# Kernel tuning notes

Hardware: AMD Instinct MI355X
Metric: run time of the kernel (lower is better)

Reference implementation:

```python
import jax, jax.numpy as jnp
import numpy as np

ALPHA = 0.5
GAMMA = 0.01
TOP_K = 5
B, T, C = 2048, 8192, 1  # C must be 1 for amp_loss's grouped conv1d to be valid


def _ashift_loss(inp, tgt):
    _, t_len, _ = inp.shape
    sm = jax.nn.softmax(inp - tgt, axis=1)                      # [B,T,C]
    return jnp.mean(jnp.sum(jnp.abs(1.0 / t_len - sm), axis=1, keepdims=True))


def _phase_loss(inp, tgt, top_k=TOP_K):
    inp_f = jnp.fft.rfft(inp, axis=1)                           # [B,Tf,C] complex
    tgt_f = jnp.fft.rfft(tgt, axis=1)
    b, tf_len, c = tgt_f.shape
    amp = jnp.abs(tgt_f).at[:, 0, :].set(0.0)                   # zero DC bin
    # top-k magnitudes along freq axis (per batch, per channel)
    _, idx = jax.lax.top_k(jnp.transpose(amp, (0, 2, 1)), top_k)  # [B,C,k]
    top = jnp.transpose(idx, (0, 2, 1))                         # [B,k,C]
    # boolean mask: True everywhere except top-k freq bins (per column)
    freqs = jnp.arange(tf_len)
    mask = ~jnp.any(freqs[None, :, None, None] == top[:, None, :, :], axis=2)  # [B,Tf,C]
    # replicate torch row-major boolean-mask flatten + view(B, Tf-k, C):
    flat = mask.reshape(b, tf_len * c)
    order = jnp.argsort(~flat, axis=1, stable=True)             # kept (True) positions first, in row-major order
    keep = order[:, : (tf_len - top_k) * c]                     # flat (t*C + c') positions
    non_top = (keep // c).reshape(b, tf_len - top_k, c)         # stored value is the freq index t
    dom = jnp.take_along_axis(tgt_f, top, axis=1) - jnp.take_along_axis(inp_f, top, axis=1)
    domain_loss = jnp.mean(jnp.sqrt(jnp.sum(jnp.abs(dom) ** 2, axis=1)))
    gath = jnp.take_along_axis(inp_f, non_top, axis=1)          # [B,Tf-k,C]
    nondomain_loss = jnp.mean(jnp.sqrt(jnp.sum(jnp.abs(gath) ** 2, axis=1, keepdims=True)))
    return domain_loss + nondomain_loss


def _amp_loss(inp, tgt):
    # Valid only for C==1: conv1d([B,1,T], weight=[B,1,T], groups=1) -> [B,B,1]
    # out[b,o] = sum_t tgt[b,t] * flip(kernel)[o,t]
    t2 = tgt[:, :, 0]                                           # [B,T]
    i2 = inp[:, :, 0]
    flip_diff = t2[:, ::-1] - i2[:, ::-1]                       # flip(target) - flip(input)
    diff = jnp.einsum('bt,ot->bo', t2, flip_diff)               # self_corr - cross_corr, [B,B]
    # torch.norm(p=2) over the singleton dim == abs
    return jnp.mean(jnp.abs(diff))


def setup_inputs() -> dict:
    key = jax.random.key(0)
    k1, k2 = jax.random.split(key)
    inp = jax.random.normal(k1, (B, T, C), dtype=jnp.float32)
    tgt = jax.random.normal(k2, (B, T, C), dtype=jnp.float32)
    return {"input": inp, "target": tgt}


def reference(input, target):
    return (ALPHA * _ashift_loss(input, target)
            + (1.0 - ALPHA) * _phase_loss(input, target)
            + GAMMA * _amp_loss(input, target))
```

## Files before the change

kernel.cpp:

```cpp
#include <hip/hip_runtime.h>
#include <hip/hip_bf16.h>
#include <math.h>

#define B_N 2048
#define T_N 8192
#define NFFT 4096
#define TF_LEN 4097
#define TOPK 5
#define KSPLIT 4
#define GBK 64

#define ZIDX(n) ((n) + ((n) >> 4) + ((n) >> 8))
#define ZPAD (NFFT + (NFFT >> 4) + (NFFT >> 8))

typedef float f32x4 __attribute__((ext_vector_type(4)));
typedef __bf16 bf16x8 __attribute__((ext_vector_type(8)));
typedef unsigned short ushort_t;

__device__ __forceinline__ void gload_lds16(const ushort_t* g, ushort_t* l) {
    __builtin_amdgcn_global_load_lds(
        (const __attribute__((address_space(1))) void*)g,
        (__attribute__((address_space(3))) void*)l,
        16, 0, 0);
}

__device__ __forceinline__ float wave_reduce_sum(float v) {
    for (int o = 32; o >= 1; o >>= 1) v += __shfl_xor(v, o, 64);
    return v;
}
__device__ __forceinline__ float wave_reduce_max(float v) {
    for (int o = 32; o >= 1; o >>= 1) v = fmaxf(v, __shfl_xor(v, o, 64));
    return v;
}

__device__ __forceinline__ ushort_t f2bf(float x) {
    __hip_bfloat16 h = __float2bfloat16(x);
    return *reinterpret_cast<ushort_t*>(&h);
}

__device__ __forceinline__ float2 cis_rev(float rev) {
    return make_float2(__builtin_amdgcn_cosf(rev), __builtin_amdgcn_sinf(rev));
}
__device__ __forceinline__ float2 cmulf(float2 a, float2 b) {
    return make_float2(a.x * b.x - a.y * b.y, a.x * b.y + a.y * b.x);
}

__device__ __forceinline__ void gen_pows(float2 w1, float2 tw[16]) {
    tw[1] = w1;
    tw[2] = cmulf(w1, w1);
    tw[3] = cmulf(tw[2], w1);
    tw[4] = cmulf(tw[2], tw[2]);
    tw[5] = cmulf(tw[4], w1);
    tw[6] = cmulf(tw[4], tw[2]);
    tw[7] = cmulf(tw[4], tw[3]);
    tw[8] = cmulf(tw[4], tw[4]);
    tw[9] = cmulf(tw[8], w1);
    tw[10] = cmulf(tw[8], tw[2]);
    tw[11] = cmulf(tw[8], tw[3]);
    tw[12] = cmulf(tw[8], tw[4]);
    tw[13] = cmulf(tw[8], tw[5]);
    tw[14] = cmulf(tw[8], tw[6]);
    tw[15] = cmulf(tw[8], tw[7]);
}

__global__ __launch_bounds__(256) void init_kernel(float* acc, float* Cpart, int nzbuf) {
    if (blockIdx.x == 0 && threadIdx.x < 4) acc[threadIdx.x] = 0.0f;
    if (nzbuf == 1) {
        size_t idx = ((size_t)blockIdx.x * 256 + threadIdx.x) * 4;
        *reinterpret_cast<f32x4*>(&Cpart[idx]) = (f32x4){0.f, 0.f, 0.f, 0.f};
    }
}

__device__ __forceinline__ void dft4(float2 x0, float2 x1, float2 x2, float2 x3,
                                     float2* y0, float2* y1, float2* y2, float2* y3) {
    float2 t0 = make_float2(x0.x + x2.x, x0.y + x2.y);
    float2 t1 = make_float2(x0.x - x2.x, x0.y - x2.y);
    float2 t2 = make_float2(x1.x + x3.x, x1.y + x3.y);
    float2 t3 = make_float2(x1.x - x3.x, x1.y - x3.y);
    *y0 = make_float2(t0.x + t2.x, t0.y + t2.y);
    *y2 = make_float2(t0.x - t2.x, t0.y - t2.y);
    *y1 = make_float2(t1.x + t3.y, t1.y - t3.x);
    *y3 = make_float2(t1.x - t3.y, t1.y + t3.x);
}

__device__ __forceinline__ void dft16(float2 X[16]) {
    float2 G[16];
    dft4(X[0], X[4], X[8],  X[12], &G[0],  &G[1],  &G[2],  &G[3]);
    dft4(X[1], X[5], X[9],  X[13], &G[4],  &G[5],  &G[6],  &G[7]);
    dft4(X[2], X[6], X[10], X[14], &G[8],  &G[9],  &G[10], &G[11]);
    dft4(X[3], X[7], X[11], X[15], &G[12], &G[13], &G[14], &G[15]);
    const float C1 = 0.9238795325112867f, S1 = 0.3826834323650898f;
    const float R2 = 0.7071067811865476f;
    G[5]  = cmulf(G[5],  make_float2(C1, -S1));
    G[6]  = cmulf(G[6],  make_float2(R2, -R2));
    G[7]  = cmulf(G[7],  make_float2(S1, -C1));
    G[9]  = cmulf(G[9],  make_float2(R2, -R2));
    { float2 g = G[10]; G[10] = make_float2(g.y, -g.x); }
    G[11] = cmulf(G[11], make_float2(-R2, -R2));
    G[13] = cmulf(G[13], make_float2(S1, -C1));
    G[14] = cmulf(G[14], make_float2(-R2, -R2));
    G[15] = cmulf(G[15], make_float2(-C1, S1));
    dft4(G[0], G[4], G[8],  G[12], &X[0], &X[4], &X[8],  &X[12]);
    dft4(G[1], G[5], G[9],  G[13], &X[1], &X[5], &X[9],  &X[13]);
    dft4(G[2], G[6], G[10], G[14], &X[2], &X[6], &X[10], &X[14]);
    dft4(G[3], G[7], G[11], G[15], &X[3], &X[7], &X[11], &X[15]);
}

__device__ __forceinline__ void rfft_bin(const float2* Zs, int k, float* orr, float* oi) {
    int kk = k & (NFFT - 1);
    int nk = (NFFT - k) & (NFFT - 1);
    float2 zk = Zs[ZIDX(kk)], znk = Zs[ZIDX(nk)];
    float xer = 0.5f * (zk.x + znk.x);
    float xei = 0.5f * (zk.y - znk.y);
    float xo_r = 0.5f * (zk.y + znk.y);
    float xo_i = -0.5f * (zk.x - znk.x);
    float2 w = cis_rev((float)k * (-1.0f / (float)T_N));
    *orr = xer + w.x * xo_r - w.y * xo_i;
    *oi = xei + w.x * xo_i + w.y * xo_r;
}

__global__ __launch_bounds__(256) void fused_row_kernel(const float* __restrict__ inp,
                                                        const float* __restrict__ tgt,
                                                        ushort_t* __restrict__ Abf,
                                                        ushort_t* __restrict__ Bbf,
                                                        float* acc) {
    __shared__ float2 Zs[ZPAD];
    __shared__ float red[12];
    __shared__ float wv[2][4];
    __shared__ int wi[2][4];
    __shared__ float2 tgtF[TOPK];
    __shared__ float rscratch[64];

    int b = blockIdx.x;
    int tid = threadIdx.x;
    int lane = tid & 63, wid = tid >> 6;
    const float* tp = tgt + (size_t)b * T_N;
    const float* ip = inp + (size_t)b * T_N;
    ushort_t* Ab = Abf + (size_t)b * T_N;
    ushort_t* Bb = Bbf + (size_t)b * T_N;

    float4 trv[8];
#pragma unroll
    for (int i = 0; i < 8; i++) {
        int q = tid + 256 * i;
        trv[i] = *reinterpret_cast<const float4*>(&tp[4 * q]);
        ushort4 ua;
        ua.x = f2bf(trv[i].x); ua.y = f2bf(trv[i].y);
        ua.z = f2bf(trv[i].z); ua.w = f2bf(trv[i].w);
        *reinterpret_cast<ushort4*>(&Ab[4 * q]) = ua;
        int m0 = 2 * q, m1 = 2 * q + 1;
        int p0 = ((m0 & 15) << 8) | (m0 & 0x0F0) | (m0 >> 8);
        int p1 = ((m1 & 15) << 8) | (m1 & 0x0F0) | (m1 >> 8);
        Zs[ZIDX(p0)] = make_float2(trv[i].x, trv[i].y);
        Zs[ZIDX(p1)] = make_float2(trv[i].z, trv[i].w);
    }

    float4 irv[8], dv[8];
#pragma unroll
    for (int i = 0; i < 8; i++) {
        int q = tid + 256 * i;
        irv[i] = *reinterpret_cast<const float4*>(&ip[4 * q]);
        dv[i] = make_float4(irv[i].x - trv[i].x, irv[i].y - trv[i].y,
                            irv[i].z - trv[i].z, irv[i].w - trv[i].w);
        ushort4 ub;
        ub.x = f2bf(-dv[i].w); ub.y = f2bf(-dv[i].z);
        ub.z = f2bf(-dv[i].y); ub.w = f2bf(-dv[i].x);
        uint2 p = *reinterpret_cast<uint2*>(&ub);
        p.x = __shfl_xor(p.x, 63, 64);
        p.y = __shfl_xor(p.y, 63, 64);
        int o = lane + 64 * (31 - wid - 4 * i);
        *reinterpret_cast<uint2*>(&Bb[4 * o]) = p;
    }

    {
        float lmax = -1e30f;
#pragma unroll
        for (int i = 0; i < 8; i++)
            lmax = fmaxf(lmax, fmaxf(fmaxf(dv[i].x, dv[i].y), fmaxf(dv[i].z, dv[i].w)));
        lmax = wave_reduce_max(lmax);
        if (lane == 0) red[wid] = lmax;
        __syncthreads();
        float mx = fmaxf(fmaxf(red[0], red[1]), fmaxf(red[2], red[3]));
        float lsum = 0.0f;
#pragma unroll
        for (int i = 0; i < 8; i++) {
            dv[i].x = __expf(dv[i].x - mx);
            dv[i].y = __expf(dv[i].y - mx);
            dv[i].z = __expf(dv[i].z - mx);
            dv[i].w = __expf(dv[i].w - mx);
            lsum += (dv[i].x + dv[i].y) + (dv[i].z + dv[i].w);
        }
        lsum = wave_reduce_sum(lsum);
        if (lane == 0) red[4 + wid] = lsum;
        __syncthreads();
        float Z = (red[4] + red[5]) + (red[6] + red[7]);
        float inv = 1.0f / Z;
        const float u = 1.0f / (float)T_N;
        float labs = 0.0f;
#pragma unroll
        for (int i = 0; i < 8; i++) {
            labs += fabsf(u - dv[i].x * inv) + fabsf(u - dv[i].y * inv) +
                    fabsf(u - dv[i].z * inv) + fabsf(u - dv[i].w * inv);
        }
        labs = wave_reduce_sum(labs);
        if (lane == 0) red[8 + wid] = labs;
        __syncthreads();
        if (tid == 0)
            atomicAdd(acc + 0, (red[8] + red[9]) + (red[10] + red[11]));
    }

    {
        float2 X[16];
        int base = tid * 16;
#pragma unroll
        for (int r = 0; r < 16; r++) X[r] = Zs[ZIDX(base + r)];
        dft16(X);
#pragma unroll
        for (int r = 0; r < 16; r++) Zs[ZIDX(base + r)] = X[r];
    }
    __syncthreads();
    {
        float2 X[16];
        int j = tid & 15;
        int base = (tid >> 4) * 256 + j;
#pragma unroll
        for (int r = 0; r < 16; r++) X[r] = Zs[ZIDX(base + 16 * r)];
        float2 tw[16];
        gen_pows(cis_rev(-(float)j * (1.0f / 256.0f)), tw);
#pragma unroll
        for (int r = 1; r < 16; r++) X[r] = cmulf(X[r], tw[r]);
        dft16(X);
#pragma unroll
        for (int r = 0; r < 16; r++) Zs[ZIDX(base + 16 * r)] = X[r];
    }
    __syncthreads();
    {
        float2 X[16];
#pragma unroll
        for (int r = 0; r < 16; r++) X[r] = Zs[ZIDX(tid + 256 * r)];
        float2 tw[16];
        gen_pows(cis_rev(-(float)tid * (1.0f / 4096.0f)), tw);
#pragma unroll
        for (int r = 1; r < 16; r++) X[r] = cmulf(X[r], tw[r]);
        dft16(X);
#pragma unroll
        for (int r = 0; r < 16; r++) Zs[ZIDX(tid + 256 * r)] = X[r];
    }
    __syncthreads();

    float av[16];
    float aN = -3.0f;
    {
        const float CC[16] = {
            1.0f, 0.9807852804032304f, 0.9238795325112867f, 0.8314696123025452f,
            0.7071067811865476f, 0.5555702330196022f, 0.3826834323650898f,
            0.1950903220161283f, 0.0f, -0.1950903220161283f, -0.3826834323650898f,
            -0.5555702330196022f, -0.7071067811865476f, -0.8314696123025452f,
            -0.9238795325112867f, -0.9807852804032304f};
        const float SS[16] = {
            0.0f, -0.1950903220161283f, -0.3826834323650898f, -0.5555702330196022f,
            -0.7071067811865476f, -0.8314696123025452f, -0.9238795325112867f,
            -0.9807852804032304f, -1.0f, -0.9807852804032304f, -0.9238795325112867f,
            -0.8314696123025452f, -0.7071067811865476f, -0.5555702330196022f,
            -0.3826834323650898f, -0.1950903220161283f};
        float2 rot0 = cis_rev(-(float)tid * (1.0f / (float)T_N));
#pragma unroll
        for (int i = 0; i < 16; i++) {
            int k = tid + 256 * i;
            if (i == 0 && tid == 0) {
                av[i] = -1.0f;
            } else {
                float2 rot = cmulf(rot0, make_float2(CC[i], SS[i]));
                int nk = (NFFT - k) & (NFFT - 1);
                float2 zk = Zs[ZIDX(k & (NFFT - 1))], znk = Zs[ZIDX(nk)];
                float xer = 0.5f * (zk.x + znk.x);
                float xei = 0.5f * (zk.y - znk.y);
                float xo_r = 0.5f * (zk.y + znk.y);
                float xo_i = -0.5f * (zk.x - znk.x);
                float xr = xer + rot.x * xo_r - rot.y * xo_i;
                float xi = xei + rot.x * xo_i + rot.y * xo_r;
                av[i] = xr * xr + xi * xi;
            }
        }
        if (tid == 0) {
            float2 z0 = Zs[ZIDX(0)];
            float v = z0.x - z0.y;
            aN = v * v;
        }
    }

    int fqa[TOPK];
#pragma unroll
    for (int r = 0; r < TOPK; r++) {
        float bv = -3.0f;
        int bi = TF_LEN;
#pragma unroll
        for (int i = 0; i < 16; i++) {
            float a = av[i];
            if (a > bv) { bv = a; bi = tid + 256 * i; }
        }
        if (aN > bv) { bv = aN; bi = 4096; }
        for (int o = 1; o < 64; o <<= 1) {
            float ov = __shfl_xor(bv, o, 64);
            int oi = __shfl_xor(bi, o, 64);
            if (ov > bv || (ov == bv && oi < bi)) { bv = ov; bi = oi; }
        }
        if (lane == 0) { wv[r & 1][wid] = bv; wi[r & 1][wid] = bi; }
        __syncthreads();
        float fv = wv[r & 1][0];
        int fi = wi[r & 1][0];
#pragma unroll
        for (int w2 = 1; w2 < 4; w2++) {
            float cv = wv[r & 1][w2];
            int ci = wi[r & 1][w2];
            if (cv > fv || (cv == fv && ci < fi)) { fv = cv; fi = ci; }
        }
        fqa[r] = fi;
        if (fi == 4096) {
            if (tid == 0) aN = -2.0f;
        } else if ((fi & 255) == tid) {
            int slot = fi >> 8;
#pragma unroll
            for (int i = 0; i < 16; i++)
                if (i == slot) av[i] = -2.0f;
        }
    }

    if (tid < TOPK) {
        int myf = fqa[0];
        if (tid == 1) myf = fqa[1];
        if (tid == 2) myf = fqa[2];
        if (tid == 3) myf = fqa[3];
        if (tid == 4) myf = fqa[4];
        float xr, xi;
        rfft_bin(Zs, myf, &xr, &xi);
        tgtF[tid] = make_float2(xr, xi);
    }
    __syncthreads();

    float2 cur[TOPK], wr[TOPK];
    float pre[TOPK][4], pim[TOPK][4];
#pragma unroll
    for (int q = 0; q < TOPK; q++) {
        int f = fqa[q];
        cur[q] = cis_rev(-(float)((f * 4 * tid) & (T_N - 1)) * (1.0f / (float)T_N));
        wr[q] = cis_rev(-(float)((f * 1024) & (T_N - 1)) * (1.0f / (float)T_N));
#pragma unroll
        for (int c = 0; c < 4; c++) { pre[q][c] = 0.0f; pim[q][c] = 0.0f; }
    }
    float E = 0.0f, sev = 0.0f, sod = 0.0f;
#pragma unroll
    for (int i = 0; i < 8; i++) {
        float4 v = irv[i];
        E = fmaf(v.x, v.x, E); sev += v.x;
        E = fmaf(v.y, v.y, E); sod += v.y;
        E = fmaf(v.z, v.z, E); sev += v.z;
        E = fmaf(v.w, v.w, E); sod += v.w;
#pragma unroll
        for (int q = 0; q < TOPK; q++) {
            pre[q][0] = fmaf(v.x, cur[q].x, pre[q][0]);
            pim[q][0] = fmaf(v.x, cur[q].y, pim[q][0]);
            pre[q][1] = fmaf(v.y, cur[q].x, pre[q][1]);
            pim[q][1] = fmaf(v.y, cur[q].y, pim[q][1]);
            pre[q][2] = fmaf(v.z, cur[q].x, pre[q][2]);
            pim[q][2] = fmaf(v.z, cur[q].y, pim[q][2]);
            pre[q][3] = fmaf(v.w, cur[q].x, pre[q][3]);
            pim[q][3] = fmaf(v.w, cur[q].y, pim[q][3]);
            cur[q] = cmulf(cur[q], wr[q]);
        }
    }
    float re[TOPK], im[TOPK];
#pragma unroll
    for (int q = 0; q < TOPK; q++) {
        float2 wcq = cis_rev(-(float)fqa[q] * (1.0f / (float)T_N));
        float tr = pre[q][3], ti = pim[q][3];
        float ur = pre[q][2] + (wcq.x * tr - wcq.y * ti);
        float ui = pim[q][2] + (wcq.x * ti + wcq.y * tr);
        float vr = pre[q][1] + (wcq.x * ur - wcq.y * ui);
        float vi = pim[q][1] + (wcq.x * ui + wcq.y * ur);
        re[q] = pre[q][0] + (wcq.x * vr - wcq.y * vi);
        im[q] = pim[q][0] + (wcq.x * vi + wcq.y * vr);
    }

    float vals[13] = {re[0], im[0], re[1], im[1], re[2], im[2], re[3], im[3],
                      re[4], im[4], E, sev + sod, sev - sod};
#pragma unroll
    for (int i = 0; i < 13; i++) {
        float v = wave_reduce_sum(vals[i]);
        if (lane == 0) rscratch[wid * 13 + i] = v;
    }
    __syncthreads();
    if (tid == 0) {
        float tot[13];
        for (int i = 0; i < 13; i++)
            tot[i] = rscratch[i] + rscratch[13 + i] + rscratch[26 + i] + rscratch[39 + i];
        float dsum = 0, isum = 0;
        for (int q = 0; q < TOPK; q++) {
            float rr = tot[2 * q], ii = tot[2 * q + 1];
            float dr = tgtF[q].x - rr, di = tgtF[q].y - ii;
            dsum += dr * dr + di * di;
            isum += rr * rr + ii * ii;
        }
        float Ee = tot[10], X0v = tot[11], Xhv = tot[12];
        float S_all = 0.5f * ((float)T_N * Ee + X0v * X0v + Xhv * Xhv);
        float val = sqrtf(dsum) + sqrtf(fmaxf(S_all - isum, 0.0f));
        atomicAdd(acc + 1, val);
    }
}

__global__ __launch_bounds__(512, 2) void gemm_kernel(const ushort_t* __restrict__ A,
                                                      const ushort_t* __restrict__ Bm,
                                                      float* __restrict__ Cpart,
                                                      int nzbuf) {
    __shared__ __align__(16) ushort_t lds[2][4][128 * 64];
    int tid = threadIdx.x;
    int bid = blockIdx.x;
    int swz = ((bid & 7) << 5) | (bid >> 3);
    int bx = swz & 7, by = (swz >> 3) & 7, bz = swz >> 6;
    int row0 = bx * 256, col0 = by * 256;
    const int KC = T_N / KSPLIT;
    const int NT = KC / GBK;
    const int NIT = NT / 2;
    int kbase = bz * KC;

    int w = tid >> 6, lane = tid & 63;
    int wm = w >> 2, wn = w & 3;
    int lr = lane & 15, kq = lane >> 4;

    f32x4 accf[8][4];
#pragma unroll
    for (int mi = 0; mi < 8; mi++)
#pragma unroll
        for (int ni = 0; ni < 4; ni++) accf[mi][ni] = (f32x4){0.f, 0.f, 0.f, 0.f};

    int strow = tid >> 3;
    int scb = (tid & 7) ^ (strow & 7);
    const ushort_t* gA0 = A + (size_t)(row0 + strow) * T_N + kbase + scb * 8;
    const ushort_t* gA1 = A + (size_t)(row0 + 128 + strow) * T_N + kbase + scb * 8;
    const ushort_t* gB0 = Bm + (size_t)(col0 + strow) * T_N + kbase + scb * 8;
    const ushort_t* gB1 = Bm + (size_t)(col0 + 128 + strow) * T_N + kbase + scb * 8;
    const size_t SUB = (size_t)64 * T_N;

    int rb0 = lr * 64 + ((kq ^ (lr & 7)) << 3);
    int rb1 = lr * 64 + (((4 + kq) ^ (lr & 7)) << 3);

#define SA_(s, buf, kt)                                                        \
    do {                                                                       \
        gload_lds16(gA0 + (s) * SUB + (size_t)(kt) * GBK, &lds[buf][0][(s) * 4096 + tid * 8]); \
        gload_lds16(gA1 + (s) * SUB + (size_t)(kt) * GBK, &lds[buf][1][(s) * 4096 + tid * 8]); \
    } while (0)
#define SB_(rg, buf, kt)                                                       \
    do {                                                                       \
        const ushort_t* g_ = ((rg) == 2) ? gB0 : gB1;                          \
        gload_lds16(g_ + (size_t)(kt) * GBK, &lds[buf][rg][tid * 8]);          \
        gload_lds16(g_ + SUB + (size_t)(kt) * GBK, &lds[buf][rg][4096 + tid * 8]); \
    } while (0)

#define PHASE(BUF, QM, QN, VMN, STAGE_STMT)                                    \
    do {                                                                       \
        asm volatile("s_waitcnt vmcnt(" #VMN ")" ::: "memory");                \
        const ushort_t* Ab_ = &lds[BUF][wm][0];                                \
        const ushort_t* Bb_ = &lds[BUF][2 + (wn >> 1)][(wn & 1) * 4096];       \
        bf16x8 a_[4][2], b_[2][2];                                             \
        _Pragma("unroll") for (int m_ = 0; m_ < 4; m_++) {                     \
            a_[m_][0] = *reinterpret_cast<const bf16x8*>(Ab_ + (QM) * 4096 + m_ * 1024 + rb0); \
            a_[m_][1] = *reinterpret_cast<const bf16x8*>(Ab_ + (QM) * 4096 + m_ * 1024 + rb1); \
        }                                                                      \
        _Pragma("unroll") for (int n_ = 0; n_ < 2; n_++) {                     \
            b_[n_][0] = *reinterpret_cast<const bf16x8*>(Bb_ + (QN) * 2048 + n_ * 1024 + rb0); \
            b_[n_][1] = *reinterpret_cast<const bf16x8*>(Bb_ + (QN) * 2048 + n_ * 1024 + rb1); \
        }                                                                      \
        STAGE_STMT;                                                            \
        __builtin_amdgcn_s_barrier();                                          \
        __builtin_amdgcn_s_setprio(1);                                         \
        _Pragma("unroll") for (int m_ = 0; m_ < 4; m_++)                       \
        _Pragma("unroll") for (int n_ = 0; n_ < 2; n_++) {                     \
            accf[(QM) * 4 + m_][(QN) * 2 + n_] = __builtin_amdgcn_mfma_f32_16x16x32_bf16( \
                a_[m_][0], b_[n_][0], accf[(QM) * 4 + m_][(QN) * 2 + n_], 0, 0, 0); \
            accf[(QM) * 4 + m_][(QN) * 2 + n_] = __builtin_amdgcn_mfma_f32_16x16x32_bf16( \
                a_[m_][1], b_[n_][1], accf[(QM) * 4 + m_][(QN) * 2 + n_], 0, 0, 0); \
        }                                                                      \
        __builtin_amdgcn_s_setprio(0);                                         \
        __builtin_amdgcn_s_barrier();                                          \
    } while (0)

    SA_(0, 0, 0);
    SA_(1, 0, 0);
    SB_(2, 0, 0);
    SB_(3, 0, 0);
    SA_(0, 1, 1);
    asm volatile("s_waitcnt vmcnt(2)" ::: "memory");
    __builtin_amdgcn_s_barrier();

    for (int it = 0; it < NIT; ++it) {
        int kt1 = 2 * it + 1;
        int te = (2 * it + 2 < NT) ? 2 * it + 2 : 2 * it;
        int to = (kt1 + 2 < NT) ? kt1 + 2 : kt1;
        PHASE(0, 0, 0, 4, SB_(3, 1, kt1));
        PHASE(0, 0, 1, 4, SB_(2, 1, kt1));
        PHASE(0, 1, 0, 6, SA_(0, 0, te));
        PHASE(0, 1, 1, 2, SA_(1, 1, kt1));
        PHASE(1, 0, 0, 4, SB_(3, 0, te));
        PHASE(1, 0, 1, 2, SB_(2, 0, te));
        PHASE(1, 1, 0, 4, SA_(1, 0, te));
        PHASE(1, 1, 1, 2, SA_(0, 1, to));
    }
#undef PHASE
#undef SA_
#undef SB_

    int crow = row0 + wm * 128 + (lane >> 4) * 4;
    int ccol = col0 + wn * 64 + lr;
    if (nzbuf == 4) {
        float* Cp = Cpart + (size_t)bz * ((size_t)B_N * B_N);
#pragma unroll
        for (int mi = 0; mi < 8; mi++)
#pragma unroll
            for (int ni = 0; ni < 4; ni++)
#pragma unroll
                for (int r = 0; r < 4; r++)
                    Cp[(size_t)(crow + mi * 16 + r) * B_N + ccol + ni * 16] =
                        accf[mi][ni][r];
    } else {
#pragma unroll
        for (int mi = 0; mi < 8; mi++)
#pragma unroll
            for (int ni = 0; ni < 4; ni++)
#pragma unroll
                for (int r = 0; r < 4; r++)
                    atomicAdd(&Cpart[(size_t)(crow + mi * 16 + r) * B_N + ccol + ni * 16],
                              accf[mi][ni][r]);
    }
}

__global__ __launch_bounds__(256) void absum_kernel(const float* __restrict__ C,
                                                    float* acc, int nzbuf) {
    __shared__ float sred[4];
    int tid = threadIdx.x;
    int lane = tid & 63, wid = tid >> 6;
    const size_t NN = (size_t)B_N * B_N;
    size_t base = (size_t)blockIdx.x * 4096;
    float s = 0.0f;
#pragma unroll
    for (int i = 0; i < 4; i++) {
        size_t idx = base + (size_t)(tid + 256 * i) * 4;
        f32x4 v = *reinterpret_cast<const f32x4*>(&C[idx]);
        if (nzbuf == 4) {
            v += *reinterpret_cast<const f32x4*>(&C[NN + idx]);
            v += *reinterpret_cast<const f32x4*>(&C[2 * NN + idx]);
            v += *reinterpret_cast<const f32x4*>(&C[3 * NN + idx]);
        }
        s += fabsf(v.x) + fabsf(v.y) + fabsf(v.z) + fabsf(v.w);
    }
    s = wave_reduce_sum(s);
    if (lane == 0) sred[wid] = s;
    __syncthreads();
    if (tid == 0) atomicAdd(acc + 2, sred[0] + sred[1] + sred[2] + sred[3]);
}

__global__ void combine_kernel(const float* acc, float* out) {
    if (threadIdx.x == 0) {
        float ash = acc[0] / (float)B_N;
        float ph = acc[1] / (float)B_N;
        float am = acc[2] / ((float)B_N * (float)B_N);
        out[0] = 0.5f * ash + 0.5f * ph + 0.01f * am;
    }
}

extern "C" void kernel_launch(void* const* d_in, const int* in_sizes, int n_in,
                              void* d_out, int out_size, void* d_ws, size_t ws_size,
                              hipStream_t stream) {
    const float* inp = (const float*)d_in[0];
    const float* tgt = (const float*)d_in[1];
    float* acc = (float*)d_ws;
    ushort_t* Abf = (ushort_t*)((char*)d_ws + 256);
    ushort_t* Bbf = Abf + (size_t)B_N * T_N;
    float* Cpart = (float*)(Bbf + (size_t)B_N * T_N);
    float* out = (float*)d_out;

    size_t need4 = 256 + 2 * (size_t)B_N * T_N * sizeof(ushort_t)
                 + (size_t)KSPLIT * (size_t)B_N * B_N * sizeof(float);
    int nzbuf = (ws_size >= need4) ? 4 : 1;

    hipLaunchKernelGGL(init_kernel, dim3(nzbuf == 1 ? 4096 : 1), dim3(256), 0, stream,
                       acc, Cpart, nzbuf);
    hipLaunchKernelGGL(fused_row_kernel, dim3(B_N), dim3(256), 0, stream,
                       inp, tgt, Abf, Bbf, acc);
    hipLaunchKernelGGL(gemm_kernel, dim3(256), dim3(512), 0, stream,
                       Abf, Bbf, Cpart, nzbuf);
    hipLaunchKernelGGL(absum_kernel, dim3(1024), dim3(256), 0, stream,
                       Cpart, acc, nzbuf);
    hipLaunchKernelGGL(combine_kernel, dim3(1), dim3(1), 0, stream, acc, out);
}
```

Measured before the change: 179.2 us.

## Fuse split-K reduction and final combine into GEMM via last-block counters

The 4-way split-K partial-sum reduction, the abs-sum and the final combine move into the GEMM kernel's epilogue. A per-tile atomic counter lets the last of the four split-K blocks for each tile reduce the partials, and a global done counter lets the final tile write the output. This removes two kernel launches and lets the reduction overlap with other GEMM blocks, where it reads from L2 while the data is still warm. The cost is extra fences and atomics, and the reduction work now falls on a subset of blocks at the tail of the GEMM.

```diff
diff --git a/kernel.cpp b/kernel.cpp
--- a/kernel.cpp
+++ b/kernel.cpp
@@ -63,8 +63,13 @@
     tw[15] = cmulf(tw[8], tw[7]);
 }
 
-__global__ __launch_bounds__(256) void init_kernel(float* acc, float* Cpart, int nzbuf) {
-    if (blockIdx.x == 0 && threadIdx.x < 4) acc[threadIdx.x] = 0.0f;
+__global__ __launch_bounds__(256) void init_kernel(float* acc, int* tcnt, int* done,
+                                                   float* Cpart, int nzbuf) {
+    if (blockIdx.x == 0) {
+        if (threadIdx.x < 4) acc[threadIdx.x] = 0.0f;
+        if (threadIdx.x >= 64 && threadIdx.x < 128) tcnt[threadIdx.x - 64] = 0;
+        if (threadIdx.x == 128) *done = 0;
+    }
     if (nzbuf == 1) {
         size_t idx = ((size_t)blockIdx.x * 256 + threadIdx.x) * 4;
         *reinterpret_cast<f32x4*>(&Cpart[idx]) = (f32x4){0.f, 0.f, 0.f, 0.f};
@@ -411,7 +416,8 @@
 __global__ __launch_bounds__(512, 2) void gemm_kernel(const ushort_t* __restrict__ A,
                                                       const ushort_t* __restrict__ Bm,
                                                       float* __restrict__ Cpart,
-                                                      int nzbuf) {
+                                                      float* acc, int* tcnt, int* done,
+                                                      float* out, int nzbuf) {
     __shared__ __align__(16) ushort_t lds[2][4][128 * 64];
     int tid = threadIdx.x;
     int bid = blockIdx.x;
@@ -512,7 +518,8 @@
     int crow = row0 + wm * 128 + (lane >> 4) * 4;
     int ccol = col0 + wn * 64 + lr;
     if (nzbuf == 4) {
-        float* Cp = Cpart + (size_t)bz * ((size_t)B_N * B_N);
+        const size_t NN = (size_t)B_N * B_N;
+        float* Cp = Cpart + (size_t)bz * NN;
 #pragma unroll
         for (int mi = 0; mi < 8; mi++)
 #pragma unroll
@@ -521,6 +528,45 @@
                 for (int r = 0; r < 4; r++)
                     Cp[(size_t)(crow + mi * 16 + r) * B_N + ccol + ni * 16] =
                         accf[mi][ni][r];
+
+        __threadfence();
+        __syncthreads();
+        int* shflag = (int*)&lds[0][0][0];
+        float* sred = (float*)&lds[0][1][0];
+        if (tid == 0) shflag[0] = atomicAdd(&tcnt[bx * 8 + by], 1);
+        __syncthreads();
+        if (shflag[0] == KSPLIT - 1) {
+            __threadfence();
+            float s = 0.0f;
+#pragma unroll
+            for (int c = 0; c < 32; c++) {
+                int idx = c * 512 + tid;
+                int row = idx >> 6;
+                int cq = idx & 63;
+                size_t off = (size_t)(row0 + row) * B_N + col0 + cq * 4;
+                f32x4 v = *reinterpret_cast<const f32x4*>(&Cpart[off]);
+                v += *reinterpret_cast<const f32x4*>(&Cpart[NN + off]);
+                v += *reinterpret_cast<const f32x4*>(&Cpart[2 * NN + off]);
+                v += *reinterpret_cast<const f32x4*>(&Cpart[3 * NN + off]);
+                s += fabsf(v.x) + fabsf(v.y) + fabsf(v.z) + fabsf(v.w);
+            }
+            s = wave_reduce_sum(s);
+            if (lane == 0) sred[w] = s;
+            __syncthreads();
+            if (tid == 0) {
+                float tot = 0.0f;
+                for (int i2 = 0; i2 < 8; i2++) tot += sred[i2];
+                atomicAdd(acc + 2, tot);
+                __threadfence();
+                int od = atomicAdd(done, 1);
+                if (od == 63) {
+                    float am = atomicAdd(acc + 2, 0.0f) / ((float)B_N * (float)B_N);
+                    float ash = acc[0] / (float)B_N;
+                    float ph = acc[1] / (float)B_N;
+                    out[0] = 0.5f * ash + 0.5f * ph + 0.01f * am;
+                }
+            }
+        }
     } else {
 #pragma unroll
         for (int mi = 0; mi < 8; mi++)
@@ -534,22 +580,16 @@
 }
 
 __global__ __launch_bounds__(256) void absum_kernel(const float* __restrict__ C,
-                                                    float* acc, int nzbuf) {
+                                                    float* acc) {
     __shared__ float sred[4];
     int tid = threadIdx.x;
     int lane = tid & 63, wid = tid >> 6;
-    const size_t NN = (size_t)B_N * B_N;
     size_t base = (size_t)blockIdx.x * 4096;
     float s = 0.0f;
 #pragma unroll
     for (int i = 0; i < 4; i++) {
         size_t idx = base + (size_t)(tid + 256 * i) * 4;
         f32x4 v = *reinterpret_cast<const f32x4*>(&C[idx]);
-        if (nzbuf == 4) {
-            v += *reinterpret_cast<const f32x4*>(&C[NN + idx]);
-            v += *reinterpret_cast<const f32x4*>(&C[2 * NN + idx]);
-            v += *reinterpret_cast<const f32x4*>(&C[3 * NN + idx]);
-        }
         s += fabsf(v.x) + fabsf(v.y) + fabsf(v.z) + fabsf(v.w);
     }
     s = wave_reduce_sum(s);
@@ -573,22 +613,25 @@
     const float* inp = (const float*)d_in[0];
     const float* tgt = (const float*)d_in[1];
     float* acc = (float*)d_ws;
-    ushort_t* Abf = (ushort_t*)((char*)d_ws + 256);
+    int* tcnt = (int*)((char*)d_ws + 256);
+    int* done = (int*)((char*)d_ws + 512);
+    ushort_t* Abf = (ushort_t*)((char*)d_ws + 1024);
     ushort_t* Bbf = Abf + (size_t)B_N * T_N;
     float* Cpart = (float*)(Bbf + (size_t)B_N * T_N);
     float* out = (float*)d_out;
 
-    size_t need4 = 256 + 2 * (size_t)B_N * T_N * sizeof(ushort_t)
+    size_t need4 = 1024 + 2 * (size_t)B_N * T_N * sizeof(ushort_t)
                  + (size_t)KSPLIT * (size_t)B_N * B_N * sizeof(float);
     int nzbuf = (ws_size >= need4) ? 4 : 1;
 
     hipLaunchKernelGGL(init_kernel, dim3(nzbuf == 1 ? 4096 : 1), dim3(256), 0, stream,
-                       acc, Cpart, nzbuf);
+                       acc, tcnt, done, Cpart, nzbuf);
     hipLaunchKernelGGL(fused_row_kernel, dim3(B_N), dim3(256), 0, stream,
                        inp, tgt, Abf, Bbf, acc);
     hipLaunchKernelGGL(gemm_kernel, dim3(256), dim3(512), 0, stream,
-                       Abf, Bbf, Cpart, nzbuf);
-    hipLaunchKernelGGL(absum_kernel, dim3(1024), dim3(256), 0, stream,
-                       Cpart, acc, nzbuf);
-    hipLaunchKernelGGL(combine_kernel, dim3(1), dim3(1), 0, stream, acc, out);
-}
+                       Abf, Bbf, Cpart, acc, tcnt, done, out, nzbuf);
+    if (nzbuf == 1) {
+        hipLaunchKernelGGL(absum_kernel, dim3(1024), dim3(256), 0, stream, Cpart, acc);
+        hipLaunchKernelGGL(combine_kernel, dim3(1), dim3(1), 0, stream, acc, out);
+    }
+}
```

New measurement: 273.0 us. +52.4%, slower.
